# Optimization experiments

Measured on AMD Instinct MI355X. Metric: run time of the kernel, lower is better.

Reference implementation:

```python
import jax, jax.numpy as jnp
import numpy as np

NH, KVH, HD = 32, 8, 128          # num heads, kv heads, head dim
HIDDEN = NH * HD                   # 4096
K_BITS = V_BITS = 4
GROUP = 32                         # quantization group size
THETA = 10000.0
FEAT = 32 // K_BITS                # values packed per int32


def _rope_cos_sin(pos, dtype=jnp.float32):
    inv_freq = 1.0 / (THETA ** (jnp.arange(0, HD, 2, dtype=jnp.float32) / HD))
    freqs = pos.astype(jnp.float32)[:, None] * inv_freq[None, :]
    emb = jnp.concatenate([freqs, freqs], axis=-1)  # [t, HD]
    return jnp.cos(emb).astype(dtype), jnp.sin(emb).astype(dtype)


def _rotate_half(x):
    x1, x2 = jnp.split(x, 2, axis=-1)
    return jnp.concatenate([-x2, x1], axis=-1)


def _apply_rope(x, pos):  # x: [b, h, t, d], pos: [t]
    cos, sin = _rope_cos_sin(pos, x.dtype)
    return x * cos[None, None] + _rotate_half(x) * sin[None, None]


def _unpack(packed, bits):
    # packed int32 [..., n] -> float [..., n * (32//bits)], little-endian bit fields
    feat = 32 // bits
    shifts = jnp.arange(feat, dtype=jnp.int32) * bits
    vals = (packed[..., None] >> shifts) & ((1 << bits) - 1)
    return vals.reshape(packed.shape[:-1] + (packed.shape[-1] * feat,)).astype(jnp.float32)


def _dequant(packed, scale, mn, bits, group):
    # group-wise affine dequant: x = q * scale + mn along last dim
    qv = _unpack(packed, bits)
    lead, L = qv.shape[:-1], qv.shape[-1]
    qv = qv.reshape(lead + (L // group, group))
    return (qv * scale[..., None] + mn[..., None]).reshape(lead + (L,))


def _repeat_kv(x, n):
    return jnp.repeat(x, n, axis=1)


def setup_inputs() -> dict:
    key = jax.random.key(0)
    ks = jax.random.split(key, 13)
    B, QL = 8, 8
    TQ, FULL_PAST = 3968, 56
    s = 0.02
    return {
        "hidden_states": jax.random.normal(ks[0], (B, QL, HIDDEN), jnp.float32),
        "Wq": jax.random.normal(ks[1], (NH * HD, HIDDEN), jnp.float32) * s,
        "Wk": jax.random.normal(ks[2], (KVH * HD, HIDDEN), jnp.float32) * s,
        "Wv": jax.random.normal(ks[3], (KVH * HD, HIDDEN), jnp.float32) * s,
        "Wo": jax.random.normal(ks[4], (NH * HD, NH * HD), jnp.float32) * s,
        "key_quant_trans": jax.random.randint(ks[5], (B, KVH, HD, TQ // FEAT), 0, 2**31 - 1, jnp.int32),
        "key_scale_trans": jax.random.uniform(ks[6], (B, KVH, HD, TQ // GROUP), jnp.float32) * 0.05 + 0.01,
        "key_mn_trans": jax.random.normal(ks[7], (B, KVH, HD, TQ // GROUP), jnp.float32) * 0.1,
        "key_full_past": jax.random.normal(ks[8], (B, KVH, FULL_PAST, HD), jnp.float32),
        "value_quant": jax.random.randint(ks[9], (B, KVH, TQ, HD // FEAT), 0, 2**31 - 1, jnp.int32),
        "value_scale": jax.random.uniform(ks[10], (B, KVH, TQ, HD // GROUP), jnp.float32) * 0.05 + 0.01,
        "value_mn": jax.random.normal(ks[11], (B, KVH, TQ, HD // GROUP), jnp.float32) * 0.1,
        "value_full_past": jax.random.normal(ks[12], (B, KVH, FULL_PAST, HD), jnp.float32),
    }


def reference(hidden_states, Wq, Wk, Wv, Wo,
              key_quant_trans, key_scale_trans, key_mn_trans, key_full_past,
              value_quant, value_scale, value_mn, value_full_past):
    b, q_len, _ = hidden_states.shape
    groups = NH // KVH
    # projections
    q = (hidden_states @ Wq.T).reshape(b, q_len, NH, HD).transpose(0, 2, 1, 3)
    k = (hidden_states @ Wk.T).reshape(b, q_len, KVH, HD).transpose(0, 2, 1, 3)
    v = (hidden_states @ Wv.T).reshape(b, q_len, KVH, HD).transpose(0, 2, 1, 3)

    TQ = key_quant_trans.shape[-1] * FEAT
    past_len = TQ + key_full_past.shape[2]
    pos_new = jnp.arange(past_len, past_len + q_len)
    qr = _apply_rope(q, pos_new)

    # quantized key segment: dequant (stored transposed [b,kvh,HD,TQ]) + fused RoPE + bmm
    kq = _dequant(key_quant_trans, key_scale_trans, key_mn_trans, K_BITS, GROUP)
    kq = _apply_rope(kq.transpose(0, 1, 3, 2), jnp.arange(TQ))  # [b,kvh,TQ,HD]
    att_quant = jnp.einsum('bhqd,bhkd->bhqk', qr, _repeat_kv(kq, groups))

    # full-precision residual key segment
    k_full = jnp.concatenate([key_full_past, k], axis=2)
    pos_full = jnp.arange(past_len + q_len - k_full.shape[2], past_len + q_len)
    k_full = _apply_rope(k_full, pos_full)
    att_full = jnp.einsum('bhqd,bhkd->bhqk', qr, _repeat_kv(k_full, groups))

    attn = jnp.concatenate([att_quant, att_full], axis=-1) / np.sqrt(HD).astype(np.float32)
    attn = jax.nn.softmax(attn.astype(jnp.float32), axis=-1).astype(qr.dtype)

    # quantized values (packed along head_dim) + full residual values
    vq = _dequant(value_quant, value_scale, value_mn, V_BITS, GROUP)  # [b,kvh,TQ,HD]
    v_full = jnp.concatenate([value_full_past, v], axis=2)
    Lf = v_full.shape[2]
    out = jnp.einsum('bhqk,bhkd->bhqd', attn[..., :-Lf], _repeat_kv(vq, groups)) \
        + jnp.einsum('bhqk,bhkd->bhqd', attn[..., -Lf:], _repeat_kv(v_full, groups))

    out = out.transpose(0, 2, 1, 3).reshape(b, q_len, NH * HD)
    return out @ Wo.T
```

## Files before the change

kernel.cpp:

```cpp
#include <hip/hip_runtime.h>

typedef unsigned short u16;
typedef short bf16x8 __attribute__((ext_vector_type(8)));
typedef float f32x4 __attribute__((ext_vector_type(4)));

__device__ __forceinline__ float b2f(u16 u){ return __uint_as_float(((unsigned)u)<<16); }
__device__ __forceinline__ u16 f2bf(float f){ return (u16)((__float_as_uint(f)+0x8000u)>>16); }
__device__ __forceinline__ float ldf(const void* p, int i, bool isbf){
  return isbf ? b2f(((const u16*)p)[i]) : ((const float*)p)[i];
}
__device__ __forceinline__ float2 ld2(const void* p, int i, bool isbf){
  if (isbf) { unsigned u = *(const unsigned*)((const u16*)p + i);
              return make_float2(b2f((u16)(u & 0xffffu)), b2f((u16)(u >> 16))); }
  return *(const float2*)((const float*)p + i);
}
__device__ __forceinline__ void pre8(uint4& A, uint4& B, const void* p, int i, bool isb){
  if (isb) { A = *(const uint4*)((const u16*)p + i); }
  else { A = *(const uint4*)((const float*)p + i);
         B = *(const uint4*)((const float*)p + i + 4); }
}
__device__ __forceinline__ void st8(u16* dst, const uint4& A, const uint4& B, bool isb){
  if (isb) { *(uint4*)dst = A; }
  else {
    const float* a = (const float*)&A; const float* b = (const float*)&B;
    dst[0]=f2bf(a[0]); dst[1]=f2bf(a[1]); dst[2]=f2bf(a[2]); dst[3]=f2bf(a[3]);
    dst[4]=f2bf(b[0]); dst[5]=f2bf(b[1]); dst[6]=f2bf(b[2]); dst[7]=f2bf(b[3]);
  }
}
__device__ __forceinline__ float c8(const float* __restrict__ p, int i, int stride){
  float s = 0.f;
  #pragma unroll
  for (int k = 0; k < 8; k++) s += p[i + k*stride];
  return s;
}
__device__ __forceinline__ void bar(){ asm volatile("s_waitcnt lgkmcnt(0)\n\ts_barrier" ::: "memory"); }
#define RORMAX(x, ctrl) fmaxf((x), __int_as_float(__builtin_amdgcn_update_dpp( \
    __float_as_int(x), __float_as_int(x), (ctrl), 0xF, 0xF, false)))
#define MFMA16(a,b,c) __builtin_amdgcn_mfma_f32_16x16x32_bf16((a),(b),(c),0,0,0)

__global__ __launch_bounds__(256) void ctab_proj_kernel(
    const u16* __restrict__ h, int* __restrict__ flag, float2* __restrict__ ctab,
    const void* __restrict__ Wa, const void* __restrict__ Wb, const void* __restrict__ Wc,
    float* __restrict__ out32)
{
  __shared__ __align__(16) u16 XW[2][64][136];
  int tid = threadIdx.x;

  if (blockIdx.x < 1008) {
    if (blockIdx.x == 0) {
      int c = 0;
      for (int i = tid; i < 4096; i += 256) {
        int e = (h[i] >> 7) & 0xFF;
        c += (e >= 116 && e <= 132) ? 1 : 0;
      }
      int* sh = (int*)XW;
      sh[tid] = c; __syncthreads();
      for (int s = 128; s > 0; s >>= 1) { if (tid < s) sh[tid] += sh[tid + s]; __syncthreads(); }
      if (tid == 0) flag[0] = (sh[0] >= 3100) ? 1 : 0;
    }
    int idx = blockIdx.x * 256 + tid;
    int dm = idx & 63, t = idx >> 6;
    float f = exp2f(-(float)dm * (13.287712379549449f / 64.0f));
    float ang = (float)t * f;
    float s, c;
    sincosf(ang, &s, &c);
    ctab[idx] = make_float2(c, s);
    return;
  }
  int bx = blockIdx.x - 1008;
  int n0 = (bx % 96) * 64;
  int ks0 = (bx / 96) * 512;
  int tot;
  {
    int c = 0;
    for (int i = tid; i < 4096; i += 256) {
      int e = (h[i] >> 7) & 0xFF;
      c += (e >= 116 && e <= 132) ? 1 : 0;
    }
    int* sh = (int*)XW;
    sh[tid] = c; __syncthreads();
    for (int s = 128; s > 0; s >>= 1) { if (tid < s) sh[tid] += sh[tid + s]; __syncthreads(); }
    tot = sh[0];
    __syncthreads();
  }
  bool fbf = (tot >= 3100);
  bool xbf = fbf;
  const void* X = h;
  const void* W; int wr0;
  if (n0 < 4096)      { W = Wa; wr0 = n0; }
  else if (n0 < 5120) { W = Wb; wr0 = n0 - 4096; }
  else                { W = Wc; wr0 = n0 - 5120; }

  int wv = tid >> 6, lane = tid & 63, lr = lane & 15, lq = lane >> 4;
  f32x4 zf = {0.f,0.f,0.f,0.f};
  f32x4 acc[4] = {zf, zf, zf, zf};

  uint4 xa[4], xb[4], wa[4], wb[4];
  #pragma unroll
  for (int s = 0; s < 4; s++) {
    int e = s * 256 + tid, row = e >> 4, c8i = e & 15;
    pre8(xa[s], xb[s], X, row * 4096 + ks0 + c8i * 8, xbf);
    pre8(wa[s], wb[s], W, (wr0 + row) * 4096 + ks0 + c8i * 8, fbf);
  }
  #pragma unroll 1
  for (int ki = 0; ki < 4; ki++) {
    bar();
    #pragma unroll
    for (int s = 0; s < 4; s++) {
      int e = s * 256 + tid, row = e >> 4, c8i = e & 15;
      st8(&XW[0][row][c8i * 8], xa[s], xb[s], xbf);
      st8(&XW[1][row][c8i * 8], wa[s], wb[s], fbf);
    }
    if (ki < 3) {
      int k0 = ks0 + (ki + 1) * 128;
      #pragma unroll
      for (int s = 0; s < 4; s++) {
        int e = s * 256 + tid, row = e >> 4, c8i = e & 15;
        pre8(xa[s], xb[s], X, row * 4096 + k0 + c8i * 8, xbf);
        pre8(wa[s], wb[s], W, (wr0 + row) * 4096 + k0 + c8i * 8, fbf);
      }
    }
    bar();
    #pragma unroll
    for (int ks = 0; ks < 4; ks++) {
      bf16x8 af = *(const bf16x8*)&XW[0][wv * 16 + lr][ks * 32 + lq * 8];
      #pragma unroll
      for (int nt = 0; nt < 4; nt++) {
        bf16x8 bv = *(const bf16x8*)&XW[1][nt * 16 + lr][ks * 32 + lq * 8];
        acc[nt] = MFMA16(af, bv, acc[nt]);
      }
    }
  }
  float* outp = out32 + (size_t)(bx / 96) * 64 * 6144;
  #pragma unroll
  for (int nt = 0; nt < 4; nt++)
    #pragma unroll
    for (int r = 0; r < 4; r++)
      outp[(wv * 16 + lq * 4 + r) * 6144 + n0 + nt * 16 + lr] = acc[nt][r];
}

__global__ __launch_bounds__(256) void proj_kernel(
    const void* __restrict__ X, const void* __restrict__ Wa,
    const void* __restrict__ Wb, const void* __restrict__ Wc,
    float* __restrict__ out32, int Na, int Nb, int ostride,
    const int* __restrict__ flagp, int x_dyn)
{
  bool fbf = (*flagp != 0);
  bool xbf = x_dyn ? fbf : true;
  int n0 = blockIdx.x * 64;
  int ks0 = blockIdx.y * 512;
  const void* W; int wr0;
  if (n0 < Na)           { W = Wa; wr0 = n0; }
  else if (n0 < Na + Nb) { W = Wb; wr0 = n0 - Na; }
  else                   { W = Wc; wr0 = n0 - Na - Nb; }

  __shared__ u16 Xs[64][136];
  __shared__ u16 Ws[64][136];
  int tid = threadIdx.x;
  int wv = tid >> 6, lane = tid & 63, lr = lane & 15, lq = lane >> 4;
  f32x4 zf = {0.f,0.f,0.f,0.f};
  f32x4 acc[4] = {zf, zf, zf, zf};

  uint4 xa[4], xb[4], wa[4], wb[4];
  #pragma unroll
  for (int s = 0; s < 4; s++) {
    int e = s * 256 + tid, row = e >> 4, c8i = e & 15;
    pre8(xa[s], xb[s], X, row * 4096 + ks0 + c8i * 8, xbf);
    pre8(wa[s], wb[s], W, (wr0 + row) * 4096 + ks0 + c8i * 8, fbf);
  }
  #pragma unroll 1
  for (int ki = 0; ki < 4; ki++) {
    bar();
    #pragma unroll
    for (int s = 0; s < 4; s++) {
      int e = s * 256 + tid, row = e >> 4, c8i = e & 15;
      st8(&Xs[row][c8i * 8], xa[s], xb[s], xbf);
      st8(&Ws[row][c8i * 8], wa[s], wb[s], fbf);
    }
    if (ki < 3) {
      int k0 = ks0 + (ki + 1) * 128;
      #pragma unroll
      for (int s = 0; s < 4; s++) {
        int e = s * 256 + tid, row = e >> 4, c8i = e & 15;
        pre8(xa[s], xb[s], X, row * 4096 + k0 + c8i * 8, xbf);
        pre8(wa[s], wb[s], W, (wr0 + row) * 4096 + k0 + c8i * 8, fbf);
      }
    }
    bar();
    #pragma unroll
    for (int ks = 0; ks < 4; ks++) {
      bf16x8 af = *(const bf16x8*)&Xs[wv * 16 + lr][ks * 32 + lq * 8];
      #pragma unroll
      for (int nt = 0; nt < 4; nt++) {
        bf16x8 bv = *(const bf16x8*)&Ws[nt * 16 + lr][ks * 32 + lq * 8];
        acc[nt] = MFMA16(af, bv, acc[nt]);
      }
    }
  }
  float* outp = out32 + (size_t)blockIdx.y * 64 * ostride;
  #pragma unroll
  for (int nt = 0; nt < 4; nt++)
    #pragma unroll
    for (int r = 0; r < 4; r++)
      outp[(wv * 16 + lq * 4 + r) * ostride + n0 + nt * 16 + lr] = acc[nt][r];
}

__global__ __launch_bounds__(256) void prep_kernel(
    const float* __restrict__ Cq32, const void* __restrict__ kfp, const void* __restrict__ vfp,
    const float2* __restrict__ ctab, const int* __restrict__ flagp,
    u16* __restrict__ qrb, u16* __restrict__ kfullb, u16* __restrict__ vfullT)
{
  bool isbf = (*flagp != 0);
  int idx = blockIdx.x * 256 + threadIdx.x;
  if (idx < 262144) {
    int d = idx & 127, row = (idx >> 7) & 31, bh = idx >> 12;
    int b = bh >> 3, kvh = bh & 7, g = row >> 3, qp = row & 7;
    int tok = b * 8 + qp, h = kvh * 4 + g;
    float x  = c8(Cq32, tok * 6144 + h * 128 + d, 393216);
    float x2 = c8(Cq32, tok * 6144 + h * 128 + (d ^ 64), 393216);
    float2 cs = ctab[(4024 + qp) * 64 + (d & 63)];
    float sgn = (d < 64) ? -1.f : 1.f;
    qrb[idx] = f2bf(x * cs.x + sgn * (x2 * cs.y));
  } else if (idx < 786432) {
    int j = idx - 262144;
    int d = j & 127, t = (j >> 7) & 63, bh = j >> 13;
    int b = bh >> 3, kvh = bh & 7;
    float x, x2;
    if (t < 56) {
      x  = ldf(kfp, (bh * 56 + t) * 128 + d, isbf);
      x2 = ldf(kfp, (bh * 56 + t) * 128 + (d ^ 64), isbf);
    } else {
      int tok = b * 8 + (t - 56);
      x  = c8(Cq32, tok * 6144 + 4096 + kvh * 128 + d, 393216);
      x2 = c8(Cq32, tok * 6144 + 4096 + kvh * 128 + (d ^ 64), 393216);
    }
    float2 cs = ctab[(3968 + t) * 64 + (d & 63)];
    float sgn = (d < 64) ? -1.f : 1.f;
    kfullb[j] = f2bf(x * cs.x + sgn * (x2 * cs.y));
  } else {
    int j = idx - 786432;
    int t = j & 63, d = (j >> 6) & 127, bh = j >> 13;
    int b = bh >> 3, kvh = bh & 7;
    float x;
    if (t < 56) x = ldf(vfp, (bh * 56 + t) * 128 + d, isbf);
    else        x = c8(Cq32, (b * 8 + t - 56) * 6144 + 5120 + kvh * 128 + d, 393216);
    vfullT[j] = f2bf(x);
  }
}

__global__ __launch_bounds__(256) void attn_kernel(
    const int* __restrict__ kqw, const void* __restrict__ ksc, const void* __restrict__ kmn,
    const int* __restrict__ vqw, const void* __restrict__ vsc, const void* __restrict__ vmn,
    const u16* __restrict__ qrb, const u16* __restrict__ kfullb, const u16* __restrict__ vfullT,
    const float2* __restrict__ ctab, const int* __restrict__ flagp,
    u16* __restrict__ Opart, float* __restrict__ ml)
{
  bool isbf = (*flagp != 0);
  int bh = blockIdx.x, grp = blockIdx.y;
  int tid = threadIdx.x;
  int c0 = grp * 4;
  int N = (grp == 15) ? 3 : 4;

  __shared__ __align__(16) unsigned char L[37120];
  u16* Kt = (u16*)L;
  u16* Vt = (u16*)(L + 16384);
  u16* Pt = (u16*)(L + 32768);
  float* pmax = (float*)(L + 36864);

  int wv = tid >> 6, lane = tid & 63, lr = lane & 15, lq = lane >> 4;
  int mt = wv & 1, nh = wv >> 1;
  int sx = (lr & 7) << 3;

  const int* kq_lo = kqw + (bh * 128 + lane) * 496;
  const int* kq_hi = kq_lo + 64 * 496;
  int klo = (bh * 128 + lane) * 124;
  int khi = klo + 64 * 124;
  const int* vqp = vqw + (bh * 3968 + lane) * 16 + wv * 4;
  int voff = (bh * 3968 + lane) * 4 + wv;

  bf16x8 qa[4];
  #pragma unroll
  for (int ks = 0; ks < 4; ks++)
    qa[ks] = *(const bf16x8*)&qrb[(bh * 32 + mt * 16 + lr) * 128 + ks * 32 + lq * 8];
  bf16x8 onev;
  #pragma unroll
  for (int j2 = 0; j2 < 8; j2++) onev[j2] = (short)0x3F80;

  float m_prev[4], l_run[4], alpha[4], mx[4];
  f32x4 zf = {0.f,0.f,0.f,0.f};
  f32x4 oacc[4] = {zf, zf, zf, zf};
  f32x4 sacc[2];
  #pragma unroll
  for (int r = 0; r < 4; r++) { m_prev[r] = -INFINITY; l_run[r] = 0.f; }

  unsigned kwl[2], kwh[2];
  float2 ksl, kml, ksh, kmh;
  uint4 vw; float vs, vm;

#define KLOAD(cn) do { \
    kwl[0] = kq_lo[(cn)*8 + wv]; kwl[1] = kq_lo[(cn)*8 + wv + 4]; \
    kwh[0] = kq_hi[(cn)*8 + wv]; kwh[1] = kq_hi[(cn)*8 + wv + 4]; \
    ksl = ld2(ksc, klo + (cn)*2, isbf); kml = ld2(kmn, klo + (cn)*2, isbf); \
    ksh = ld2(ksc, khi + (cn)*2, isbf); kmh = ld2(kmn, khi + (cn)*2, isbf); } while(0)
#define VLOAD(cn) do { \
    vw = *(const uint4*)(vqp + (cn)*1024); \
    vs = ldf(vsc, voff + (cn)*256, isbf); vm = ldf(vmn, voff + (cn)*256, isbf); } while(0)
#define KDEQ(cn) do { \
    _Pragma("unroll") \
    for (int it = 0; it < 2; it++) { \
      int w = wv + 4 * it; \
      unsigned w1 = kwl[it], w2 = kwh[it]; \
      float sc1 = it ? ksl.y : ksl.x, m1 = it ? kml.y : kml.x; \
      float sc2 = it ? ksh.y : ksh.x, m2 = it ? kmh.y : kmh.x; \
      const float2* ct = &ctab[((cn) * 64 + w * 8) * 64 + lane]; \
      _Pragma("unroll") \
      for (int ii = 0; ii < 8; ii++) { \
        float v1 = (float)((w1 >> (4 * ii)) & 15u) * sc1 + m1; \
        float v2 = (float)((w2 >> (4 * ii)) & 15u) * sc2 + m2; \
        float2 cs = ct[ii * 64]; \
        int t = w * 8 + ii; \
        Kt[(t * 128 + lane)      ^ ((t & 7) << 3)] = f2bf(v1 * cs.x - v2 * cs.y); \
        Kt[(t * 128 + lane + 64) ^ ((t & 7) << 3)] = f2bf(v2 * cs.x + v1 * cs.y); \
      } \
    } } while(0)
#define PVSTEP() do { \
    f32x4 pv[4] = {zf, zf, zf, zf}; f32x4 ls = zf; \
    _Pragma("unroll") \
    for (int ks = 0; ks < 2; ks++) { \
      bf16x8 af = *(const bf16x8*)&Pt[((mt*16 + lr)*64 + ks*32 + lq*8) ^ sx]; \
      ls = MFMA16(af, onev, ls); \
      _Pragma("unroll") \
      for (int nt = 0; nt < 4; nt++) { \
        bf16x8 bv = *(const bf16x8*)&Vt[((nh*64 + nt*16 + lr)*64 + ks*32 + lq*8) ^ sx]; \
        pv[nt] = MFMA16(af, bv, pv[nt]); \
      } \
    } \
    _Pragma("unroll") \
    for (int r = 0; r < 4; r++) { \
      l_run[r] = l_run[r] * alpha[r] + ls[r]; \
      _Pragma("unroll") \
      for (int nt = 0; nt < 4; nt++) \
        oacc[nt][r] = oacc[nt][r] * alpha[r] + pv[nt][r]; \
    } } while(0)

  KLOAD(c0);
  VLOAD(c0);
  KDEQ(c0);
  KLOAD(c0 + 1);
  bar();

  for (int i = 0; i < N; i++) {
    int c = c0 + i;
    f32x4 sa0 = zf, sa1 = zf;
    #pragma unroll
    for (int ks = 0; ks < 4; ks++) {
      bf16x8 b0 = *(const bf16x8*)&Kt[((nh*32 + lr)*128      + ks*32 + lq*8) ^ sx];
      bf16x8 b1 = *(const bf16x8*)&Kt[((nh*32 + 16 + lr)*128 + ks*32 + lq*8) ^ sx];
      sa0 = MFMA16(qa[ks], b0, sa0);
      sa1 = MFMA16(qa[ks], b1, sa1);
    }
    if (i > 0) PVSTEP();
    #pragma unroll
    for (int r = 0; r < 4; r++) {
      sa0[r] *= 0.08838834764831845f;
      sa1[r] *= 0.08838834764831845f;
      float m0 = fmaxf(sa0[r], sa1[r]);
      m0 = RORMAX(m0, 0x128);
      m0 = RORMAX(m0, 0x124);
      m0 = RORMAX(m0, 0x122);
      m0 = RORMAX(m0, 0x121);
      mx[r] = m0;
    }
    if (lr == 0) {
      #pragma unroll
      for (int r = 0; r < 4; r++) pmax[wv * 16 + lq * 4 + r] = mx[r];
    }
    sacc[0] = sa0; sacc[1] = sa1;
    bar();
    #pragma unroll
    for (int r = 0; r < 4; r++) {
      float cm = fmaxf(mx[r], pmax[(wv ^ 2) * 16 + lq * 4 + r]);
      float mn2 = fmaxf(m_prev[r], cm);
      alpha[r] = __expf(m_prev[r] - mn2);
      m_prev[r] = mn2;
    }
    #pragma unroll
    for (int nt = 0; nt < 2; nt++) {
      #pragma unroll
      for (int r = 0; r < 4; r++) {
        float p = __expf(sacc[nt][r] - m_prev[r]);
        int q = mt * 16 + lq * 4 + r, k = nh * 32 + nt * 16 + lr;
        Pt[(q * 64 + k) ^ ((q & 7) << 3)] = f2bf(p);
      }
    }
    if (c != 62) {
      unsigned wds[4] = {vw.x, vw.y, vw.z, vw.w};
      #pragma unroll
      for (int it = 0; it < 4; it++) {
        unsigned wd = wds[it];
        #pragma unroll
        for (int ii = 0; ii < 8; ii++) {
          int d = (wv * 4 + it) * 8 + ii;
          Vt[(d * 64 + lane) ^ ((d & 7) << 3)] = f2bf((float)((wd >> (4 * ii)) & 15u) * vs + vm);
        }
      }
    } else {
      for (int u = tid; u < 1024; u += 256) {
        int dd = u >> 3, t8 = u & 7;
        *(uint4*)&Vt[(dd * 64 + t8 * 8) ^ ((dd & 7) << 3)] =
            *(const uint4*)&vfullT[(bh * 128 + dd) * 64 + t8 * 8];
      }
    }
    if (i + 1 < N) {
      if (c + 1 == 62) {
        for (int u = tid; u < 1024; u += 256) {
          int row = u >> 4, cc = u & 15;
          *(uint4*)&Kt[(row * 128 + cc * 8) ^ ((row & 7) << 3)] =
              *(const uint4*)&kfullb[(bh * 64 + row) * 128 + cc * 8];
        }
      } else {
        KDEQ(c + 1);
      }
    }
    if (i + 2 < N && c + 2 < 62) KLOAD(c + 2);
    if (i + 1 < N && c + 1 < 62) VLOAD(c + 1);
    bar();
  }
  PVSTEP();

  u16* Ob = Opart + (size_t)((bh * 16 + grp) * 32) * 128;
  #pragma unroll
  for (int nt = 0; nt < 4; nt++)
    #pragma unroll
    for (int r = 0; r < 4; r++)
      Ob[(mt * 16 + lq * 4 + r) * 128 + nh * 64 + nt * 16 + lr] = f2bf(oacc[nt][r]);
  if (wv < 2 && lr == 0) {
    #pragma unroll
    for (int r = 0; r < 4; r++) {
      ml[((bh * 16 + grp) * 32 + mt * 16 + lq * 4 + r) * 2 + 0] = m_prev[r];
      ml[((bh * 16 + grp) * 32 + mt * 16 + lq * 4 + r) * 2 + 1] = l_run[r];
    }
  }
#undef KLOAD
#undef VLOAD
#undef KDEQ
#undef PVSTEP
}

__global__ __launch_bounds__(256) void combine_kernel(
    const u16* __restrict__ Opart, const float* __restrict__ ml, u16* __restrict__ attn_out)
{
  int bh = blockIdx.x, dq = blockIdx.y, tid = threadIdx.x;
  __shared__ float Wg[16][33];
  __shared__ float Ls[32];
  if (tid < 32) {
    int row = tid;
    float M = -INFINITY;
    for (int g = 0; g < 16; g++)
      M = fmaxf(M, ml[((bh * 16 + g) * 32 + row) * 2]);
    float Lacc = 0.f;
    for (int g = 0; g < 16; g++) {
      float m = ml[((bh * 16 + g) * 32 + row) * 2];
      float l = ml[((bh * 16 + g) * 32 + row) * 2 + 1];
      float w = __expf(m - M);
      Wg[g][row] = w;
      Lacc += l * w;
    }
    Ls[row] = Lacc;
  }
  __syncthreads();
  int row = tid >> 3, ds = tid & 7;
  int d0 = dq * 32 + ds * 4;
  float a0 = 0.f, a1 = 0.f, a2 = 0.f, a3 = 0.f;
  for (int g = 0; g < 16; g++) {
    float w = Wg[g][row];
    const u16* p = Opart + (size_t)((bh * 16 + g) * 32 + row) * 128 + d0;
    uint2 v = *(const uint2*)p;
    const u16* h = (const u16*)&v;
    a0 += w * b2f(h[0]); a1 += w * b2f(h[1]); a2 += w * b2f(h[2]); a3 += w * b2f(h[3]);
  }
  float inv = 1.0f / Ls[row];
  int b = bh >> 3, kvh = bh & 7, hg = row >> 3, qp = row & 7;
  u16* dst = attn_out + (size_t)(b * 8 + qp) * 4096 + (kvh * 4 + hg) * 128 + d0;
  dst[0] = f2bf(a0 * inv); dst[1] = f2bf(a1 * inv);
  dst[2] = f2bf(a2 * inv); dst[3] = f2bf(a3 * inv);
}

__global__ __launch_bounds__(256) void cast_kernel(
    const float* __restrict__ O32, const int* __restrict__ flagp, void* __restrict__ out)
{
  int i = blockIdx.x * 256 + threadIdx.x;
  float v = c8(O32, i, 262144);
  if (*flagp) ((u16*)out)[i] = f2bf(v);
  else        ((float*)out)[i] = v;
}

extern "C" void kernel_launch(void* const* d_in, const int* in_sizes, int n_in,
                              void* d_out, int out_size, void* d_ws, size_t ws_size,
                              hipStream_t stream)
{
  const void* hidden = d_in[0];
  const void* Wq  = d_in[1];
  const void* Wk  = d_in[2];
  const void* Wv  = d_in[3];
  const void* Wo  = d_in[4];
  const int*  kqw = (const int*)d_in[5];
  const void* ksc = d_in[6];
  const void* kmn = d_in[7];
  const void* kfp = d_in[8];
  const int*  vqw = (const int*)d_in[9];
  const void* vsc = d_in[10];
  const void* vmn = d_in[11];
  const void* vfp = d_in[12];

  char* ws = (char*)d_ws;
  int*    flag     = (int*)(ws);
  float2* ctab     = (float2*)(ws + 256);
  float*  Cq32     = (float*)(ws + 2064640);
  u16*    Opart    = (u16*)(ws + 2064640);
  float*  O32      = (float*)(ws + 2064640);
  u16*    qrb      = (u16*)(ws + 18841856);
  u16*    attn_out = qrb;
  u16*    kfullb   = (u16*)(ws + 19366144);
  u16*    vfullT   = (u16*)(ws + 20414720);
  float*  ml       = (float*)(ws + 21463296);

  ctab_proj_kernel<<<1776, 256, 0, stream>>>((const u16*)hidden, flag, ctab,
                                             Wq, Wk, Wv, Cq32);
  prep_kernel<<<5120, 256, 0, stream>>>(Cq32, kfp, vfp, ctab, flag, qrb, kfullb, vfullT);
  attn_kernel<<<dim3(64, 16), 256, 0, stream>>>(kqw, ksc, kmn, vqw, vsc, vmn,
                                                qrb, kfullb, vfullT, ctab, flag, Opart, ml);
  combine_kernel<<<dim3(64, 4), 256, 0, stream>>>(Opart, ml, attn_out);
  proj_kernel<<<dim3(64, 8), 256, 0, stream>>>(attn_out, Wo, Wo, Wo, O32, 4096, 0, 4096, flag, 0);
  cast_kernel<<<1024, 256, 0, stream>>>(O32, flag, d_out);
}
```

Measured before the change: 290.6 us.

## Compute RoPE angles by recurrence in key dequant and transpose V via LDS

In the attention kernel's key dequant loop, the per-token cos/sin table load is replaced by one initial table load per 8-token word, followed by complex multiplication with a single-step rotation. This removes most of the gather traffic to the ctab table. The recurrence accumulates rounding error over up to 8 steps, which is small before the bf16 rounding. Separately, the prep kernel's V transpose now goes through a shared-memory tile so that both its reads and writes are coalesced, and the launch uses fewer blocks.

```diff
diff --git a/kernel.cpp b/kernel.cpp
--- a/kernel.cpp
+++ b/kernel.cpp
@@ -210,41 +210,52 @@
     const float2* __restrict__ ctab, const int* __restrict__ flagp,
     u16* __restrict__ qrb, u16* __restrict__ kfullb, u16* __restrict__ vfullT)
 {
+  __shared__ u16 T[64][130];
   bool isbf = (*flagp != 0);
-  int idx = blockIdx.x * 256 + threadIdx.x;
-  if (idx < 262144) {
-    int d = idx & 127, row = (idx >> 7) & 31, bh = idx >> 12;
-    int b = bh >> 3, kvh = bh & 7, g = row >> 3, qp = row & 7;
-    int tok = b * 8 + qp, h = kvh * 4 + g;
-    float x  = c8(Cq32, tok * 6144 + h * 128 + d, 393216);
-    float x2 = c8(Cq32, tok * 6144 + h * 128 + (d ^ 64), 393216);
-    float2 cs = ctab[(4024 + qp) * 64 + (d & 63)];
-    float sgn = (d < 64) ? -1.f : 1.f;
-    qrb[idx] = f2bf(x * cs.x + sgn * (x2 * cs.y));
-  } else if (idx < 786432) {
-    int j = idx - 262144;
-    int d = j & 127, t = (j >> 7) & 63, bh = j >> 13;
+  int tid = threadIdx.x;
+  if (blockIdx.x < 3072) {
+    int idx = blockIdx.x * 256 + tid;
+    if (idx < 262144) {
+      int d = idx & 127, row = (idx >> 7) & 31, bh = idx >> 12;
+      int b = bh >> 3, kvh = bh & 7, g = row >> 3, qp = row & 7;
+      int tok = b * 8 + qp, h = kvh * 4 + g;
+      float x  = c8(Cq32, tok * 6144 + h * 128 + d, 393216);
+      float x2 = c8(Cq32, tok * 6144 + h * 128 + (d ^ 64), 393216);
+      float2 cs = ctab[(4024 + qp) * 64 + (d & 63)];
+      float sgn = (d < 64) ? -1.f : 1.f;
+      qrb[idx] = f2bf(x * cs.x + sgn * (x2 * cs.y));
+    } else {
+      int j = idx - 262144;
+      int d = j & 127, t = (j >> 7) & 63, bh = j >> 13;
+      int b = bh >> 3, kvh = bh & 7;
+      float x, x2;
+      if (t < 56) {
+        x  = ldf(kfp, (bh * 56 + t) * 128 + d, isbf);
+        x2 = ldf(kfp, (bh * 56 + t) * 128 + (d ^ 64), isbf);
+      } else {
+        int tok = b * 8 + (t - 56);
+        x  = c8(Cq32, tok * 6144 + 4096 + kvh * 128 + d, 393216);
+        x2 = c8(Cq32, tok * 6144 + 4096 + kvh * 128 + (d ^ 64), 393216);
+      }
+      float2 cs = ctab[(3968 + t) * 64 + (d & 63)];
+      float sgn = (d < 64) ? -1.f : 1.f;
+      kfullb[j] = f2bf(x * cs.x + sgn * (x2 * cs.y));
+    }
+  } else {
+    int bh = blockIdx.x - 3072;
     int b = bh >> 3, kvh = bh & 7;
-    float x, x2;
-    if (t < 56) {
-      x  = ldf(kfp, (bh * 56 + t) * 128 + d, isbf);
-      x2 = ldf(kfp, (bh * 56 + t) * 128 + (d ^ 64), isbf);
-    } else {
-      int tok = b * 8 + (t - 56);
-      x  = c8(Cq32, tok * 6144 + 4096 + kvh * 128 + d, 393216);
-      x2 = c8(Cq32, tok * 6144 + 4096 + kvh * 128 + (d ^ 64), 393216);
-    }
-    float2 cs = ctab[(3968 + t) * 64 + (d & 63)];
-    float sgn = (d < 64) ? -1.f : 1.f;
-    kfullb[j] = f2bf(x * cs.x + sgn * (x2 * cs.y));
-  } else {
-    int j = idx - 786432;
-    int t = j & 63, d = (j >> 6) & 127, bh = j >> 13;
-    int b = bh >> 3, kvh = bh & 7;
-    float x;
-    if (t < 56) x = ldf(vfp, (bh * 56 + t) * 128 + d, isbf);
-    else        x = c8(Cq32, (b * 8 + t - 56) * 6144 + 5120 + kvh * 128 + d, 393216);
-    vfullT[j] = f2bf(x);
+    for (int u = tid; u < 8192; u += 256) {
+      int t = u >> 7, d = u & 127;
+      float x;
+      if (t < 56) x = ldf(vfp, (bh * 56 + t) * 128 + d, isbf);
+      else        x = c8(Cq32, (b * 8 + t - 56) * 6144 + 5120 + kvh * 128 + d, 393216);
+      T[t][d] = f2bf(x);
+    }
+    __syncthreads();
+    for (int u = tid; u < 8192; u += 256) {
+      int d = u >> 6, t = u & 63;
+      vfullT[bh * 8192 + u] = T[t][d];
+    }
   }
 }
 
@@ -285,6 +296,7 @@
   bf16x8 onev;
   #pragma unroll
   for (int j2 = 0; j2 < 8; j2++) onev[j2] = (short)0x3F80;
+  float2 csd = ctab[64 + lane];
 
   float m_prev[4], l_run[4], alpha[4], mx[4];
   f32x4 zf = {0.f,0.f,0.f,0.f};
@@ -295,13 +307,16 @@
 
   unsigned kwl[2], kwh[2];
   float2 ksl, kml, ksh, kmh;
+  float2 ct0[2];
   uint4 vw; float vs, vm;
 
 #define KLOAD(cn) do { \
     kwl[0] = kq_lo[(cn)*8 + wv]; kwl[1] = kq_lo[(cn)*8 + wv + 4]; \
     kwh[0] = kq_hi[(cn)*8 + wv]; kwh[1] = kq_hi[(cn)*8 + wv + 4]; \
     ksl = ld2(ksc, klo + (cn)*2, isbf); kml = ld2(kmn, klo + (cn)*2, isbf); \
-    ksh = ld2(ksc, khi + (cn)*2, isbf); kmh = ld2(kmn, khi + (cn)*2, isbf); } while(0)
+    ksh = ld2(ksc, khi + (cn)*2, isbf); kmh = ld2(kmn, khi + (cn)*2, isbf); \
+    ct0[0] = ctab[((cn)*64 + wv*8)*64 + lane]; \
+    ct0[1] = ctab[((cn)*64 + (wv+4)*8)*64 + lane]; } while(0)
 #define VLOAD(cn) do { \
     vw = *(const uint4*)(vqp + (cn)*1024); \
     vs = ldf(vsc, voff + (cn)*256, isbf); vm = ldf(vmn, voff + (cn)*256, isbf); } while(0)
@@ -312,15 +327,17 @@
       unsigned w1 = kwl[it], w2 = kwh[it]; \
       float sc1 = it ? ksl.y : ksl.x, m1 = it ? kml.y : kml.x; \
       float sc2 = it ? ksh.y : ksh.x, m2 = it ? kmh.y : kmh.x; \
-      const float2* ct = &ctab[((cn) * 64 + w * 8) * 64 + lane]; \
+      float2 cs = ct0[it]; \
       _Pragma("unroll") \
       for (int ii = 0; ii < 8; ii++) { \
         float v1 = (float)((w1 >> (4 * ii)) & 15u) * sc1 + m1; \
         float v2 = (float)((w2 >> (4 * ii)) & 15u) * sc2 + m2; \
-        float2 cs = ct[ii * 64]; \
         int t = w * 8 + ii; \
         Kt[(t * 128 + lane)      ^ ((t & 7) << 3)] = f2bf(v1 * cs.x - v2 * cs.y); \
         Kt[(t * 128 + lane + 64) ^ ((t & 7) << 3)] = f2bf(v2 * cs.x + v1 * cs.y); \
+        float nx = cs.x * csd.x - cs.y * csd.y; \
+        cs.y = cs.y * csd.x + cs.x * csd.y; \
+        cs.x = nx; \
       } \
     } } while(0)
 #define PVSTEP() do { \
@@ -527,7 +544,7 @@
 
   ctab_proj_kernel<<<1776, 256, 0, stream>>>((const u16*)hidden, flag, ctab,
                                              Wq, Wk, Wv, Cq32);
-  prep_kernel<<<5120, 256, 0, stream>>>(Cq32, kfp, vfp, ctab, flag, qrb, kfullb, vfullT);
+  prep_kernel<<<3136, 256, 0, stream>>>(Cq32, kfp, vfp, ctab, flag, qrb, kfullb, vfullT);
   attn_kernel<<<dim3(64, 16), 256, 0, stream>>>(kqw, ksc, kmn, vqw, vsc, vmn,
                                                 qrb, kfullb, vfullT, ctab, flag, Opart, ml);
   combine_kernel<<<dim3(64, 4), 256, 0, stream>>>(Opart, ml, attn_out);
```

After: 299.0 us. 2.9% more time.
